# Optimization experiments

Hardware: AMD Instinct MI355X
Metric: run time of the kernel (lower is better)

Reference implementation:

```python
import jax, jax.numpy as jnp
import numpy as np

EPS = 1e-16  # matches PyG softmax denominator epsilon


def setup_inputs() -> dict:
    key = jax.random.key(0)
    k1, k2, k3, k4 = jax.random.split(key, 4)
    N, F, G = 200000, 256, 1024
    x = jax.random.normal(k1, (N, F), dtype=jnp.float32)
    batch = jnp.sort(jax.random.randint(k2, (N,), 0, G, dtype=jnp.int64))
    Wg = jax.random.normal(k3, (F, 1), dtype=jnp.float32) / np.sqrt(F)
    bg = jnp.zeros((1,), dtype=jnp.float32)
    Wn = jax.random.normal(k4, (F, F), dtype=jnp.float32) / np.sqrt(F)
    bn = jnp.zeros((F,), dtype=jnp.float32)
    return {"x": x, "batch": batch, "size": G, "Wg": Wg, "bg": bg, "Wn": Wn, "bn": bn}


def reference(x, batch, size, Wg, bg, Wn, bn):
    # gate scores: [N, 1]
    gate = x @ Wg + bg
    # transformed features: [N, F]
    h = x @ Wn + bn
    # per-graph (segment) softmax over gate, numerically stable
    seg_max = jax.ops.segment_max(gate, batch, num_segments=size)  # [G, 1]
    e = jnp.exp(gate - seg_max[batch])                             # [N, 1]
    seg_sum = jax.ops.segment_sum(e, batch, num_segments=size)     # [G, 1]
    alpha = e / (seg_sum[batch] + EPS)                             # [N, 1]
    # weighted scatter-add: [G, F]
    out = jax.ops.segment_sum(alpha * h, batch, num_segments=size)
    return out
```

## Files before the change

### kernel.cpp

```cpp
#include <hip/hip_runtime.h>
#include <math.h>

#define FDIM 256
#define EPSF 1e-16f
#define K4_ROWS 2

typedef float f32x4 __attribute__((ext_vector_type(4)));

__device__ __forceinline__ float dot4v(f32x4 a, f32x4 b) {
    return a.x * b.x + a.y * b.y + a.z * b.z + a.w * b.w;
}

__device__ __forceinline__ f32x4 ntload(const float* p) {
    return __builtin_nontemporal_load(reinterpret_cast<const f32x4*>(p));
}

__global__ void __launch_bounds__(256) k_ranges(const int* __restrict__ batch,
                                                int* __restrict__ seg_start,
                                                int N, int G) {
    int i = blockIdx.x * blockDim.x + threadIdx.x;
    if (i > N) return;
    int b  = (i == N) ? G : batch[i];
    int bp = (i == 0) ? -1 : batch[i - 1];
    for (int g = bp + 1; g <= b; ++g) seg_start[g] = i;
}

__global__ void __launch_bounds__(256) k_fused(const int* __restrict__ seg_start,
                                               const float* __restrict__ x,
                                               const float* __restrict__ Wg,
                                               float* __restrict__ yp,
                                               float* __restrict__ sp) {
    int b = blockIdx.x;
    int g = b >> 1, half = b & 1;
    int s0 = seg_start[g];
    int e0 = seg_start[g + 1];
    int mid = s0 + ((e0 - s0) >> 1);
    int rs = half ? mid : s0;
    int re = half ? e0 : mid;

    __shared__ float s_s[16];
    __shared__ float s_acc[16][FDIM];

    int wave = threadIdx.x >> 6;
    int group = (threadIdx.x >> 4) & 3;
    int l16 = threadIdx.x & 15;
    int part = (wave << 2) | group;

    const f32x4 wg0 = *reinterpret_cast<const f32x4*>(Wg +   0 + l16 * 4);
    const f32x4 wg1 = *reinterpret_cast<const f32x4*>(Wg +  64 + l16 * 4);
    const f32x4 wg2 = *reinterpret_cast<const f32x4*>(Wg + 128 + l16 * 4);
    const f32x4 wg3 = *reinterpret_cast<const f32x4*>(Wg + 192 + l16 * 4);

    f32x4 a0 = (f32x4)0.f, a1 = (f32x4)0.f, a2 = (f32x4)0.f, a3 = (f32x4)0.f;
    float s = 0.f;

    int r = rs + part;
    for (; r + 16 < re; r += 32) {
        const float* rp0 = x + (size_t)r * FDIM;
        const float* rp1 = x + (size_t)(r + 16) * FDIM;
        f32x4 x0 = ntload(rp0 +   0 + l16 * 4);
        f32x4 x1 = ntload(rp0 +  64 + l16 * 4);
        f32x4 x2 = ntload(rp0 + 128 + l16 * 4);
        f32x4 x3 = ntload(rp0 + 192 + l16 * 4);
        f32x4 y0 = ntload(rp1 +   0 + l16 * 4);
        f32x4 y1 = ntload(rp1 +  64 + l16 * 4);
        f32x4 y2 = ntload(rp1 + 128 + l16 * 4);
        f32x4 y3 = ntload(rp1 + 192 + l16 * 4);
        float d0 = dot4v(x0, wg0) + dot4v(x1, wg1) + dot4v(x2, wg2) + dot4v(x3, wg3);
        float d1 = dot4v(y0, wg0) + dot4v(y1, wg1) + dot4v(y2, wg2) + dot4v(y3, wg3);
        #pragma unroll
        for (int off = 1; off < 16; off <<= 1) {
            d0 += __shfl_xor(d0, off, 64);
            d1 += __shfl_xor(d1, off, 64);
        }
        float w0 = __expf(d0);
        float w1 = __expf(d1);
        a0 += w0 * x0; a1 += w0 * x1; a2 += w0 * x2; a3 += w0 * x3;
        a0 += w1 * y0; a1 += w1 * y1; a2 += w1 * y2; a3 += w1 * y3;
        s += w0 + w1;
    }
    if (r < re) {
        const float* rp = x + (size_t)r * FDIM;
        f32x4 x0 = ntload(rp +   0 + l16 * 4);
        f32x4 x1 = ntload(rp +  64 + l16 * 4);
        f32x4 x2 = ntload(rp + 128 + l16 * 4);
        f32x4 x3 = ntload(rp + 192 + l16 * 4);
        float d = dot4v(x0, wg0) + dot4v(x1, wg1) + dot4v(x2, wg2) + dot4v(x3, wg3);
        #pragma unroll
        for (int off = 1; off < 16; off <<= 1) d += __shfl_xor(d, off, 64);
        float w = __expf(d);
        a0 += w * x0; a1 += w * x1; a2 += w * x2; a3 += w * x3;
        s += w;
    }

    *reinterpret_cast<f32x4*>(&s_acc[part][  0 + l16 * 4]) = a0;
    *reinterpret_cast<f32x4*>(&s_acc[part][ 64 + l16 * 4]) = a1;
    *reinterpret_cast<f32x4*>(&s_acc[part][128 + l16 * 4]) = a2;
    *reinterpret_cast<f32x4*>(&s_acc[part][192 + l16 * 4]) = a3;
    if (l16 == 0) s_s[part] = s;
    __syncthreads();

    int c = threadIdx.x;
    float v = 0.f;
    #pragma unroll
    for (int p = 0; p < 16; ++p) v += s_acc[p][c];
    yp[(size_t)b * FDIM + c] = v;
    if (threadIdx.x == 0) {
        float t = 0.f;
        #pragma unroll
        for (int p = 0; p < 16; ++p) t += s_s[p];
        sp[b] = t;
    }
}

__global__ void __launch_bounds__(256) k4_out(const float* __restrict__ yp,
                                              const float* __restrict__ sp,
                                              const float* __restrict__ Wn,
                                              const float* __restrict__ bn,
                                              float* __restrict__ out, int G) {
    int g0 = blockIdx.x * K4_ROWS;
    __shared__ float ys[K4_ROWS][FDIM];
    __shared__ float s_alpha[K4_ROWS];
    int c = threadIdx.x;
    #pragma unroll
    for (int r = 0; r < K4_ROWS; ++r) {
        int g = g0 + r;
        if (g < G) {
            float sg = sp[2 * g] + sp[2 * g + 1];
            float inv = 1.0f / (sg + EPSF);
            ys[r][c] = (yp[(size_t)(2 * g) * FDIM + c] +
                        yp[(size_t)(2 * g + 1) * FDIM + c]) * inv;
            if (c == 0) s_alpha[r] = sg * inv;
        } else {
            ys[r][c] = 0.f;
            if (c == 0) s_alpha[r] = 0.f;
        }
    }
    __syncthreads();
    float acc[K4_ROWS];
    #pragma unroll
    for (int r = 0; r < K4_ROWS; ++r) acc[r] = 0.f;
    #pragma unroll 8
    for (int k = 0; k < FDIM; ++k) {
        float w = Wn[k * FDIM + c];
        #pragma unroll
        for (int r = 0; r < K4_ROWS; ++r) acc[r] += ys[r][k] * w;
    }
    float bv = bn[c];
    #pragma unroll
    for (int r = 0; r < K4_ROWS; ++r) {
        int g = g0 + r;
        if (g < G) out[(size_t)g * FDIM + c] = acc[r] + s_alpha[r] * bv;
    }
}

extern "C" void kernel_launch(void* const* d_in, const int* in_sizes, int n_in,
                              void* d_out, int out_size, void* d_ws, size_t ws_size,
                              hipStream_t stream) {
    const float* x     = (const float*)d_in[0];
    const int*   batch = (const int*)d_in[1];
    const float* Wg    = (const float*)d_in[3];
    const float* Wn    = (const float*)d_in[5];
    const float* bn    = (const float*)d_in[6];
    float* out = (float*)d_out;

    int N = in_sizes[1];
    int G = out_size / FDIM;

    int*   seg_start = (int*)d_ws;
    float* sp = (float*)(seg_start + ((G + 2) & ~1));
    float* yp = sp + 2 * G;

    k_ranges<<<(N + 1 + 255) / 256, 256, 0, stream>>>(batch, seg_start, N, G);
    k_fused<<<2 * G, 256, 0, stream>>>(seg_start, x, Wg, yp, sp);
    k4_out<<<(G + K4_ROWS - 1) / K4_ROWS, 256, 0, stream>>>(yp, sp, Wn, bn, out, G);
}
```

Baseline: 49.15 us.

## Use one 512-thread block per segment and retile the output GEMV

The fused reduction kernel now runs one 512-thread block per graph instead of two 256-thread half-segment blocks. It normalizes by the softmax sum in-kernel and writes the normalized pooled row plus alpha directly. The final projection kernel is restructured so each 512-thread block covers 8 graphs by 64 output columns, reading yn rows directly from global memory instead of staging them in shared memory. This removes the partial-sum combine step, but shared memory per block roughly doubles (32x256 floats), which may reduce occupancy.

```diff
diff --git a/kernel.cpp b/kernel.cpp
--- a/kernel.cpp
+++ b/kernel.cpp
@@ -3,7 +3,6 @@
 
 #define FDIM 256
 #define EPSF 1e-16f
-#define K4_ROWS 2
 
 typedef float f32x4 __attribute__((ext_vector_type(4)));
 
@@ -25,26 +24,20 @@
     for (int g = bp + 1; g <= b; ++g) seg_start[g] = i;
 }
 
-__global__ void __launch_bounds__(256) k_fused(const int* __restrict__ seg_start,
+__global__ void __launch_bounds__(512) k_fused(const int* __restrict__ seg_start,
                                                const float* __restrict__ x,
                                                const float* __restrict__ Wg,
-                                               float* __restrict__ yp,
-                                               float* __restrict__ sp) {
-    int b = blockIdx.x;
-    int g = b >> 1, half = b & 1;
-    int s0 = seg_start[g];
-    int e0 = seg_start[g + 1];
-    int mid = s0 + ((e0 - s0) >> 1);
-    int rs = half ? mid : s0;
-    int re = half ? e0 : mid;
+                                               float* __restrict__ yn,
+                                               float* __restrict__ alpha) {
+    int g = blockIdx.x;
+    int rs = seg_start[g];
+    int re = seg_start[g + 1];
 
-    __shared__ float s_s[16];
-    __shared__ float s_acc[16][FDIM];
+    __shared__ float s_s[32];
+    __shared__ float s_acc[32][FDIM];
 
-    int wave = threadIdx.x >> 6;
-    int group = (threadIdx.x >> 4) & 3;
-    int l16 = threadIdx.x & 15;
-    int part = (wave << 2) | group;
+    int part = threadIdx.x >> 4;
+    int l16  = threadIdx.x & 15;
 
     const f32x4 wg0 = *reinterpret_cast<const f32x4*>(Wg +   0 + l16 * 4);
     const f32x4 wg1 = *reinterpret_cast<const f32x4*>(Wg +  64 + l16 * 4);
@@ -55,9 +48,9 @@
     float s = 0.f;
 
     int r = rs + part;
-    for (; r + 16 < re; r += 32) {
+    for (; r + 32 < re; r += 64) {
         const float* rp0 = x + (size_t)r * FDIM;
-        const float* rp1 = x + (size_t)(r + 16) * FDIM;
+        const float* rp1 = x + (size_t)(r + 32) * FDIM;
         f32x4 x0 = ntload(rp0 +   0 + l16 * 4);
         f32x4 x1 = ntload(rp0 +  64 + l16 * 4);
         f32x4 x2 = ntload(rp0 + 128 + l16 * 4);
@@ -100,58 +93,38 @@
     if (l16 == 0) s_s[part] = s;
     __syncthreads();
 
-    int c = threadIdx.x;
-    float v = 0.f;
-    #pragma unroll
-    for (int p = 0; p < 16; ++p) v += s_acc[p][c];
-    yp[(size_t)b * FDIM + c] = v;
-    if (threadIdx.x == 0) {
-        float t = 0.f;
+    if (threadIdx.x < FDIM) {
+        int c = threadIdx.x;
+        float v = 0.f;
         #pragma unroll
-        for (int p = 0; p < 16; ++p) t += s_s[p];
-        sp[b] = t;
+        for (int p = 0; p < 32; ++p) v += s_acc[p][c];
+        float tot = 0.f;
+        #pragma unroll
+        for (int p = 0; p < 32; ++p) tot += s_s[p];
+        float inv = 1.0f / (tot + EPSF);
+        yn[(size_t)g * FDIM + c] = v * inv;
+        if (c == 0) alpha[g] = tot * inv;
     }
 }
 
-__global__ void __launch_bounds__(256) k4_out(const float* __restrict__ yp,
-                                              const float* __restrict__ sp,
-                                              const float* __restrict__ Wn,
-                                              const float* __restrict__ bn,
-                                              float* __restrict__ out, int G) {
-    int g0 = blockIdx.x * K4_ROWS;
-    __shared__ float ys[K4_ROWS][FDIM];
-    __shared__ float s_alpha[K4_ROWS];
-    int c = threadIdx.x;
-    #pragma unroll
-    for (int r = 0; r < K4_ROWS; ++r) {
-        int g = g0 + r;
-        if (g < G) {
-            float sg = sp[2 * g] + sp[2 * g + 1];
-            float inv = 1.0f / (sg + EPSF);
-            ys[r][c] = (yp[(size_t)(2 * g) * FDIM + c] +
-                        yp[(size_t)(2 * g + 1) * FDIM + c]) * inv;
-            if (c == 0) s_alpha[r] = sg * inv;
-        } else {
-            ys[r][c] = 0.f;
-            if (c == 0) s_alpha[r] = 0.f;
-        }
-    }
-    __syncthreads();
-    float acc[K4_ROWS];
-    #pragma unroll
-    for (int r = 0; r < K4_ROWS; ++r) acc[r] = 0.f;
+__global__ void __launch_bounds__(512) k4s(const float* __restrict__ yn,
+                                           const float* __restrict__ alpha,
+                                           const float* __restrict__ Wn,
+                                           const float* __restrict__ bn,
+                                           float* __restrict__ out, int G) {
+    int bx = blockIdx.x & 3;
+    int by = blockIdx.x >> 2;
+    int r = threadIdx.x >> 6;
+    int c = bx * 64 + (threadIdx.x & 63);
+    int g = by * 8 + r;
+    if (g >= G) return;
+    const float* yrow = yn + (size_t)g * FDIM;
+    const float* wcol = Wn + c;
+    float acc = 0.f;
     #pragma unroll 8
-    for (int k = 0; k < FDIM; ++k) {
-        float w = Wn[k * FDIM + c];
-        #pragma unroll
-        for (int r = 0; r < K4_ROWS; ++r) acc[r] += ys[r][k] * w;
-    }
-    float bv = bn[c];
-    #pragma unroll
-    for (int r = 0; r < K4_ROWS; ++r) {
-        int g = g0 + r;
-        if (g < G) out[(size_t)g * FDIM + c] = acc[r] + s_alpha[r] * bv;
-    }
+    for (int k = 0; k < FDIM; ++k)
+        acc = fmaf(yrow[k], wcol[(size_t)k * FDIM], acc);
+    out[(size_t)g * FDIM + c] = acc + alpha[g] * bn[c];
 }
 
 extern "C" void kernel_launch(void* const* d_in, const int* in_sizes, int n_in,
@@ -168,10 +141,10 @@
     int G = out_size / FDIM;
 
     int*   seg_start = (int*)d_ws;
-    float* sp = (float*)(seg_start + ((G + 2) & ~1));
-    float* yp = sp + 2 * G;
+    float* alpha = (float*)(seg_start + ((G + 2) & ~1));
+    float* yn = alpha + G;
 
     k_ranges<<<(N + 1 + 255) / 256, 256, 0, stream>>>(batch, seg_start, N, G);
-    k_fused<<<2 * G, 256, 0, stream>>>(seg_start, x, Wg, yp, sp);
-    k4_out<<<(G + K4_ROWS - 1) / K4_ROWS, 256, 0, stream>>>(yp, sp, Wn, bn, out, G);
+    k_fused<<<G, 512, 0, stream>>>(seg_start, x, Wg, yn, alpha);
+    k4s<<<((G + 7) / 8) * 4, 512, 0, stream>>>(yn, alpha, Wn, bn, out, G);
 }
```

New measurement: 58.63 us. 1.19x slower.
